# Performance work log

Hardware: AMD Instinct MI355X
Metric: run time of the kernel (lower is better)

## Reference

```python
import jax, jax.numpy as jnp
import numpy as np

S, B, D, K, E = 2048, 16, 256, 2048, 1048576  # seq_len, batch, input_dim, max_seq_len, n_edges


def setup_inputs() -> dict:
    key = jax.random.key(0)
    k1, k2, k3, k4, k5 = jax.random.split(key, 5)
    M = jax.random.normal(k1, (S, B, D), dtype=jnp.float32)
    W = jax.random.normal(k2, (K, D), dtype=jnp.float32) * (1.0 / np.sqrt(D))
    lengths = jax.random.randint(k3, (B,), 1, S, dtype=jnp.int64)
    edge_batch = jax.random.randint(k4, (E,), 0, B, dtype=jnp.int64)
    edge_ij = jax.random.randint(k5, (E, 2), 0, K, dtype=jnp.int64)
    return {"M": M, "W": W, "lengths": lengths, "edge_batch": edge_batch, "edge_ij": edge_ij}


def reference(M, W, lengths, edge_batch, edge_ij):
    # scale = Linear(input_dim, max_seq_len, bias=False): (S, B, K)
    scale = jnp.einsum('sbd,kd->sbk', M, W)
    # softmax over the sequence dim (dim=0), then permute(1,2,0) -> (B, K, S)
    alpha = jnp.transpose(jax.nn.softmax(scale, axis=0), (1, 2, 0))
    # mask = ones*1e-10 with edges set to 1; mask_copy = zeros with edges set to 1
    mask = jnp.full(alpha.shape, 1e-10, dtype=alpha.dtype)
    mask = mask.at[edge_batch, edge_ij[:, 0], edge_ij[:, 1]].set(1.0)
    mask_copy = jnp.zeros(alpha.shape, dtype=alpha.dtype)
    mask_copy = mask_copy.at[edge_batch, edge_ij[:, 0], edge_ij[:, 1]].set(1.0)
    masked_alpha = alpha * mask
    sums = masked_alpha.sum(-1, keepdims=True)
    scores = (masked_alpha / sums) * mask_copy
    return scores
```

## Files before the change

### kernel.cpp

```cpp
#include <hip/hip_runtime.h>

#define S_LEN 2048
#define B_DIM 16
#define D_DIM 256
#define K_DIM 2048
#define E_NUM 1048576

typedef __attribute__((ext_vector_type(4))) float f32x4;
typedef __attribute__((ext_vector_type(8))) short s16x8;
typedef __attribute__((ext_vector_type(4))) unsigned short u16x4;

__device__ __forceinline__ unsigned short f2bf(float f) {
    unsigned int u = __float_as_uint(f);
    u += 0x7fffu + ((u >> 16) & 1u);
    return (unsigned short)(u >> 16);
}

__global__ void prep_kernel(const float* __restrict__ W, const float* __restrict__ M,
                            unsigned short* __restrict__ Wbf, unsigned short* __restrict__ Mbf,
                            unsigned long long* __restrict__ mw) {
    int bid = blockIdx.x;
    if (bid < 2048) {
        int t = bid * 256 + threadIdx.x;
        ((f32x4*)mw)[t] = (f32x4){0.f, 0.f, 0.f, 0.f};
    } else if (bid < 2560) {
        int t = (bid - 2048) * 256 + threadIdx.x;
        f32x4 v = ((const f32x4*)W)[t];
        u16x4 u;
        u.x = f2bf(v.x); u.y = f2bf(v.y); u.z = f2bf(v.z); u.w = f2bf(v.w);
        ((u16x4*)Wbf)[t] = u;
    } else {
        int t = (bid - 2560) * 256 + threadIdx.x;
        f32x4 v = ((const f32x4*)M)[t];
        int flat4 = t * 4;
        int d0 = flat4 & 255;
        int sb = flat4 >> 8;
        int b  = sb & 15;
        int s  = sb >> 4;
        u16x4 u;
        u.x = f2bf(v.x); u.y = f2bf(v.y); u.z = f2bf(v.z); u.w = f2bf(v.w);
        *(u16x4*)&Mbf[((size_t)(b * S_LEN + s)) * D_DIM + d0] = u;
    }
}

__global__ void maskbuild_kernel(const int* __restrict__ eb, const int* __restrict__ ij,
                                 unsigned long long* __restrict__ mw) {
    int e = blockIdx.x * 256 + threadIdx.x;
    int b = eb[e];
    int2 p = *(const int2*)&ij[2 * e];
    size_t w = ((size_t)(b * K_DIM + p.x)) * 32 + (p.y >> 6);
    atomicOr(&mw[w], 1ull << (p.y & 63));
}

__launch_bounds__(256, 2)
__global__ void gemm8_kernel(const unsigned short* __restrict__ Mbf,
                             const unsigned short* __restrict__ Wbf,
                             const unsigned long long* __restrict__ mw,
                             float* __restrict__ out) {
    __shared__ unsigned short Msh[2][64 * 256];
    __shared__ float smZ[4][4][16];
    __shared__ float smE[4][4][16];

    const int tid  = threadIdx.x;
    const int x    = blockIdx.x;
    const int b    = ((x & 7) << 1) | ((x >> 3) & 1);
    const int k0   = (x >> 4) * 64;
    const int lane = tid & 63;
    const int w    = tid >> 6;
    const int r    = lane & 15;
    const int g    = lane >> 4;

    const unsigned short* MB = Mbf + (size_t)b * S_LEN * D_DIM;
    const size_t mrow = (size_t)(b * K_DIM + k0 + r) * 32;

    s16x8 breg[4][8];
    #pragma unroll
    for (int ks = 0; ks < 4; ++ks)
        #pragma unroll
        for (int d = 0; d < 8; ++d)
            breg[ks][d] = *(const s16x8*)&Wbf[(size_t)(k0 + ks * 16 + r) * D_DIM + d * 32 + g * 8];

    const int lrh  = lane >> 5;
    const int lc16 = lane & 31;

    auto stage = [&](int bufi, int t) {
        const int s0 = t * 64;
        unsigned short* buf = &Msh[bufi][0];
        #pragma unroll
        for (int c = 0; c < 8; ++c) {
            const int row   = w * 16 + c * 2 + lrh;
            const int col16 = lc16 ^ (row & 7);
            const unsigned short* src = MB + (size_t)(s0 + row) * D_DIM + col16 * 8;
            char* dst = (char*)buf + w * 8192 + c * 1024;
            __builtin_amdgcn_global_load_lds(
                (__attribute__((address_space(1))) const void*)src,
                (__attribute__((address_space(3))) void*)dst, 16, 0, 0);
        }
    };

    float Zl[4]  = {0.f, 0.f, 0.f, 0.f};
    float Zel[4] = {0.f, 0.f, 0.f, 0.f};

    stage(0, 0);
    __syncthreads();

    for (int t = 0; t < 32; ++t) {
        if (t < 31) stage((t & 1) ^ 1, t + 1);
        unsigned long long wv[4];
        #pragma unroll
        for (int ks = 0; ks < 4; ++ks) wv[ks] = mw[mrow + ks * 512 + t];
        const unsigned short* cur = &Msh[t & 1][0];

        f32x4 acc[4];
        #pragma unroll
        for (int ks = 0; ks < 4; ++ks) acc[ks] = (f32x4){0.f, 0.f, 0.f, 0.f};

        #pragma unroll
        for (int d = 0; d < 8; ++d) {
            const int acol = ((d * 4 + g) ^ (r & 7)) * 8;
            s16x8 a = *(const s16x8*)&cur[(w * 16 + r) * 256 + acol];
            #pragma unroll
            for (int ks = 0; ks < 4; ++ks)
                acc[ks] = __builtin_amdgcn_mfma_f32_16x16x32_bf16(a, breg[ks][d], acc[ks], 0, 0, 0);
        }

        const int sh = w * 16 + g * 4;
        #pragma unroll
        for (int ks = 0; ks < 4; ++ks) {
            #pragma unroll
            for (int rr = 0; rr < 4; ++rr) {
                float e = __expf(acc[ks][rr]);
                Zl[ks] += e;
                Zel[ks] += ((wv[ks] >> (sh + rr)) & 1ull) ? e : 0.f;
            }
        }
        __syncthreads();
    }

    #pragma unroll
    for (int ks = 0; ks < 4; ++ks) {
        Zl[ks]  += __shfl_xor(Zl[ks], 16);  Zl[ks]  += __shfl_xor(Zl[ks], 32);
        Zel[ks] += __shfl_xor(Zel[ks], 16); Zel[ks] += __shfl_xor(Zel[ks], 32);
    }
    if (g == 0) {
        #pragma unroll
        for (int ks = 0; ks < 4; ++ks) { smZ[w][ks][r] = Zl[ks]; smE[w][ks][r] = Zel[ks]; }
    }
    stage(0, 0);
    __syncthreads();

    float rdv[4];
    #pragma unroll
    for (int ks = 0; ks < 4; ++ks) {
        float Z  = smZ[0][ks][r] + smZ[1][ks][r] + smZ[2][ks][r] + smZ[3][ks][r];
        float Ze = smE[0][ks][r] + smE[1][ks][r] + smE[2][ks][r] + smE[3][ks][r];
        rdv[ks] = 1.0f / (1e-10f * (Z - Ze) + Ze);
    }

    for (int t = 0; t < 32; ++t) {
        if (t < 31) stage((t & 1) ^ 1, t + 1);
        unsigned long long wv[4];
        #pragma unroll
        for (int ks = 0; ks < 4; ++ks) wv[ks] = mw[mrow + ks * 512 + t];
        const unsigned short* cur = &Msh[t & 1][0];

        f32x4 acc[4];
        #pragma unroll
        for (int ks = 0; ks < 4; ++ks) acc[ks] = (f32x4){0.f, 0.f, 0.f, 0.f};

        #pragma unroll
        for (int d = 0; d < 8; ++d) {
            const int acol = ((d * 4 + g) ^ (r & 7)) * 8;
            s16x8 a = *(const s16x8*)&cur[(w * 16 + r) * 256 + acol];
            #pragma unroll
            for (int ks = 0; ks < 4; ++ks)
                acc[ks] = __builtin_amdgcn_mfma_f32_16x16x32_bf16(a, breg[ks][d], acc[ks], 0, 0, 0);
        }

        const int sh = w * 16 + g * 4;
        #pragma unroll
        for (int ks = 0; ks < 4; ++ks) {
            f32x4 ov;
            #pragma unroll
            for (int rr = 0; rr < 4; ++rr) {
                bool edge = (wv[ks] >> (sh + rr)) & 1ull;
                ov[rr] = edge ? __expf(acc[ks][rr]) * rdv[ks] : 0.f;
            }
            *(f32x4*)&out[(size_t)(b * K_DIM + k0 + ks * 16 + r) * S_LEN
                          + t * 64 + w * 16 + g * 4] = ov;
        }
        __syncthreads();
    }
}

extern "C" void kernel_launch(void* const* d_in, const int* in_sizes, int n_in,
                              void* d_out, int out_size, void* d_ws, size_t ws_size,
                              hipStream_t stream) {
    (void)in_sizes; (void)n_in; (void)ws_size; (void)out_size;
    const float* M  = (const float*)d_in[0];
    const float* W  = (const float*)d_in[1];
    const int* eb   = (const int*)d_in[3];
    const int* ij   = (const int*)d_in[4];
    float* out      = (float*)d_out;
    char* ws        = (char*)d_ws;

    unsigned long long* mw = (unsigned long long*)ws;
    unsigned short* Wbf = (unsigned short*)(ws + 8388608);
    unsigned short* Mbf = (unsigned short*)(ws + 9437184);

    prep_kernel<<<10752, 256, 0, stream>>>(W, M, Wbf, Mbf, mw);
    maskbuild_kernel<<<E_NUM / 256, 256, 0, stream>>>(eb, ij, mw);
    gemm8_kernel<<<512, 256, 0, stream>>>(Mbf, Wbf, mw, out);
}
```

Baseline: 198.4 us.

## Replace second GEMM pass with sparse normalization kernel over edge bits

The fused kernel no longer recomputes the whole GEMM and exp in a second pass. It writes the unnormalized masked exp values in the first pass and stores per-row reciprocal normalizers to workspace. A new finalize kernel walks the edge bitmask and rescales only the edge entries in place. The per-iteration __syncthreads is also dropped, since each wave stages and reads only its own rows. This trades half the MFMA and exp work for a sparse read-modify-write pass and a reliance on intra-wave ordering of the LDS loads.

```diff
diff --git a/kernel.cpp b/kernel.cpp
--- a/kernel.cpp
+++ b/kernel.cpp
@@ -53,10 +53,11 @@
 }
 
 __launch_bounds__(256, 2)
-__global__ void gemm8_kernel(const unsigned short* __restrict__ Mbf,
-                             const unsigned short* __restrict__ Wbf,
-                             const unsigned long long* __restrict__ mw,
-                             float* __restrict__ out) {
+__global__ void gemm12_kernel(const unsigned short* __restrict__ Mbf,
+                              const unsigned short* __restrict__ Wbf,
+                              const unsigned long long* __restrict__ mw,
+                              float* __restrict__ rd,
+                              float* __restrict__ out) {
     __shared__ unsigned short Msh[2][64 * 256];
     __shared__ float smZ[4][4][16];
     __shared__ float smE[4][4][16];
@@ -102,7 +103,6 @@
     float Zel[4] = {0.f, 0.f, 0.f, 0.f};
 
     stage(0, 0);
-    __syncthreads();
 
     for (int t = 0; t < 32; ++t) {
         if (t < 31) stage((t & 1) ^ 1, t + 1);
@@ -127,14 +127,18 @@
         const int sh = w * 16 + g * 4;
         #pragma unroll
         for (int ks = 0; ks < 4; ++ks) {
+            f32x4 ov;
             #pragma unroll
             for (int rr = 0; rr < 4; ++rr) {
                 float e = __expf(acc[ks][rr]);
                 Zl[ks] += e;
-                Zel[ks] += ((wv[ks] >> (sh + rr)) & 1ull) ? e : 0.f;
+                bool edge = (wv[ks] >> (sh + rr)) & 1ull;
+                Zel[ks] += edge ? e : 0.f;
+                ov[rr] = edge ? e : 0.f;
             }
-        }
-        __syncthreads();
+            *(f32x4*)&out[(size_t)(b * K_DIM + k0 + ks * 16 + r) * S_LEN
+                          + t * 64 + w * 16 + g * 4] = ov;
+        }
     }
 
     #pragma unroll
@@ -146,50 +150,33 @@
         #pragma unroll
         for (int ks = 0; ks < 4; ++ks) { smZ[w][ks][r] = Zl[ks]; smE[w][ks][r] = Zel[ks]; }
     }
-    stage(0, 0);
     __syncthreads();
-
-    float rdv[4];
-    #pragma unroll
-    for (int ks = 0; ks < 4; ++ks) {
-        float Z  = smZ[0][ks][r] + smZ[1][ks][r] + smZ[2][ks][r] + smZ[3][ks][r];
-        float Ze = smE[0][ks][r] + smE[1][ks][r] + smE[2][ks][r] + smE[3][ks][r];
-        rdv[ks] = 1.0f / (1e-10f * (Z - Ze) + Ze);
-    }
-
-    for (int t = 0; t < 32; ++t) {
-        if (t < 31) stage((t & 1) ^ 1, t + 1);
-        unsigned long long wv[4];
-        #pragma unroll
-        for (int ks = 0; ks < 4; ++ks) wv[ks] = mw[mrow + ks * 512 + t];
-        const unsigned short* cur = &Msh[t & 1][0];
-
-        f32x4 acc[4];
-        #pragma unroll
-        for (int ks = 0; ks < 4; ++ks) acc[ks] = (f32x4){0.f, 0.f, 0.f, 0.f};
-
-        #pragma unroll
-        for (int d = 0; d < 8; ++d) {
-            const int acol = ((d * 4 + g) ^ (r & 7)) * 8;
-            s16x8 a = *(const s16x8*)&cur[(w * 16 + r) * 256 + acol];
-            #pragma unroll
-            for (int ks = 0; ks < 4; ++ks)
-                acc[ks] = __builtin_amdgcn_mfma_f32_16x16x32_bf16(a, breg[ks][d], acc[ks], 0, 0, 0);
-        }
-
-        const int sh = w * 16 + g * 4;
+    if (w == 0 && g == 0) {
         #pragma unroll
         for (int ks = 0; ks < 4; ++ks) {
-            f32x4 ov;
-            #pragma unroll
-            for (int rr = 0; rr < 4; ++rr) {
-                bool edge = (wv[ks] >> (sh + rr)) & 1ull;
-                ov[rr] = edge ? __expf(acc[ks][rr]) * rdv[ks] : 0.f;
-            }
-            *(f32x4*)&out[(size_t)(b * K_DIM + k0 + ks * 16 + r) * S_LEN
-                          + t * 64 + w * 16 + g * 4] = ov;
-        }
-        __syncthreads();
+            float Z  = smZ[0][ks][r] + smZ[1][ks][r] + smZ[2][ks][r] + smZ[3][ks][r];
+            float Ze = smE[0][ks][r] + smE[1][ks][r] + smE[2][ks][r] + smE[3][ks][r];
+            rd[b * K_DIM + k0 + ks * 16 + r] = 1.0f / (1e-10f * (Z - Ze) + Ze);
+        }
+    }
+}
+
+__global__ void finalize_kernel(const unsigned long long* __restrict__ mw,
+                                const float* __restrict__ rd,
+                                float* __restrict__ out) {
+    const int p    = blockIdx.x;
+    const int b    = ((p & 7) << 1) | ((p >> 3) & 1);
+    const int rest = p >> 4;
+    const int t    = (b << 16) + (rest << 8) + threadIdx.x;
+    unsigned long long bits = mw[t];
+    if (!bits) return;
+    const int row = t >> 5;
+    const float rdv = rd[row];
+    const size_t base = (size_t)row * S_LEN + (t & 31) * 64;
+    while (bits) {
+        const int j = __builtin_ctzll(bits);
+        bits &= bits - 1;
+        out[base + j] *= rdv;
     }
 }
 
@@ -207,8 +194,10 @@
     unsigned long long* mw = (unsigned long long*)ws;
     unsigned short* Wbf = (unsigned short*)(ws + 8388608);
     unsigned short* Mbf = (unsigned short*)(ws + 9437184);
+    float* rd = (float*)(ws + 26214400);
 
     prep_kernel<<<10752, 256, 0, stream>>>(W, M, Wbf, Mbf, mw);
     maskbuild_kernel<<<E_NUM / 256, 256, 0, stream>>>(eb, ij, mw);
-    gemm8_kernel<<<512, 256, 0, stream>>>(Mbf, Wbf, mw, out);
-}
+    gemm12_kernel<<<512, 256, 0, stream>>>(Mbf, Wbf, mw, rd, out);
+    finalize_kernel<<<4096, 256, 0, stream>>>(mw, rd, out);
+}
```

Result: faster. 187.6 us (-5.4%).
